# Optimization experiments

Measured on AMD Instinct MI355X. Metric: run time of the kernel, lower is better.

## Reference

```python
import jax, jax.numpy as jnp
import numpy as np

B, Q_LEN, HIST = 1, 2048, 2048
H, KVH, D, HID = 12, 2, 128, 1536
GROUPS = H // KVH  # 6
THETA = 1000000.0


def setup_inputs() -> dict:
    key = jax.random.key(0)
    ks = jax.random.split(key, 8)
    x = jax.random.normal(ks[0], (B, Q_LEN, HID), jnp.float32)
    Wq = jax.random.normal(ks[1], (HID, HID), jnp.float32) * 0.02
    bq = jnp.zeros((HID,), jnp.float32)
    Wk = jax.random.normal(ks[2], (HID, KVH * D), jnp.float32) * 0.02
    bk = jnp.zeros((KVH * D,), jnp.float32)
    Wv = jax.random.normal(ks[3], (HID, KVH * D), jnp.float32) * 0.02
    bv = jnp.zeros((KVH * D,), jnp.float32)
    Wo = jax.random.normal(ks[4], (HID, HID), jnp.float32) * 0.02
    k_hist = jax.random.normal(ks[5], (B, HIST, KVH, D), jnp.float32)
    v_hist = jax.random.normal(ks[6], (B, HIST, KVH, D), jnp.float32)
    # RoPE angles for current-chunk positions [HIST, HIST+Q_LEN)
    inv_freq = 1.0 / (THETA ** (jnp.arange(0, D, 2, dtype=jnp.float32) / D))  # [D/2]
    t = jnp.arange(HIST, HIST + Q_LEN, dtype=jnp.float32)
    ang = t[:, None] * inv_freq[None, :]  # [Q_LEN, D/2]
    return dict(x=x, Wq=Wq, bq=bq, Wk=Wk, bk=bk, Wv=Wv, bv=bv, Wo=Wo,
                k_hist=k_hist, v_hist=v_hist,
                freqs_cos=jnp.cos(ang), freqs_sin=jnp.sin(ang))


def apply_rope(x, cos, sin):
    # x: [B, S, H, D]; cos/sin: [S, D/2]. Split-half rotation (matches torch.polar impl).
    half = D // 2
    x1, x2 = x[..., :half], x[..., half:]
    c = cos[None, :, None, :]
    s = sin[None, :, None, :]
    return jnp.concatenate([x1 * c - x2 * s, x1 * s + x2 * c], axis=-1)


def reference(x, Wq, bq, Wk, bk, Wv, bv, Wo, k_hist, v_hist, freqs_cos, freqs_sin):
    q = (x @ Wq + bq).reshape(B, Q_LEN, H, D)
    k = (x @ Wk + bk).reshape(B, Q_LEN, KVH, D)
    v = (x @ Wv + bv).reshape(B, Q_LEN, KVH, D)
    q = apply_rope(q, freqs_cos, freqs_sin)
    k = apply_rope(k, freqs_cos, freqs_sin)
    # KV-cache concat along sequence dim
    k = jnp.concatenate([k_hist, k], axis=1)  # [B, K_LEN, KVH, D]
    v = jnp.concatenate([v_hist, v], axis=1)
    k_len = HIST + Q_LEN
    # GQA: repeat kv heads (repeat_interleave equivalent along head axis)
    k = jnp.repeat(k, GROUPS, axis=2)  # [B, K_LEN, H, D]
    v = jnp.repeat(v, GROUPS, axis=2)
    scores = jnp.einsum('bqhd,bkhd->bhqk', q, k) / jnp.sqrt(jnp.float32(D))
    # causal mask: triu(-inf, diagonal=k_len - q_len + 1)
    qi = jnp.arange(Q_LEN)[:, None]
    ki = jnp.arange(k_len)[None, :]
    mask = jnp.where(ki > qi + (k_len - Q_LEN), jnp.float32(-jnp.inf), 0.0)
    scores = scores + mask[None, None]
    probs = jax.nn.softmax(scores, axis=-1)
    out = jnp.einsum('bhqk,bkhd->bqhd', probs, v).reshape(B, Q_LEN, HID)
    return out @ Wo
```

## Files before the change

### kernel.cpp

```cpp
#include <hip/hip_runtime.h>
#include <math.h>

#define QL 2048
#define HISTN 2048
#define KLEN 4096
#define NH 12
#define NKVH 2
#define HD 128
#define HID 1536
#define NQKV 2048
#define VTROWS 144
#define QSCALE 0.08838834764831845f

typedef unsigned short u16;
typedef short bf16x8 __attribute__((ext_vector_type(8)));
typedef float f32x4 __attribute__((ext_vector_type(4)));

__device__ __forceinline__ u16 f2bf(float f) {
  union { float f; unsigned u; } v; v.f = f;
  unsigned r = v.u + 0x7FFFu + ((v.u >> 16) & 1u);
  return (u16)(r >> 16);
}
__device__ __forceinline__ float bf2f(u16 h) {
  union { unsigned u; float f; } v; v.u = ((unsigned)h) << 16; return v.f;
}
__device__ __forceinline__ unsigned cvt_pk_bf16(float lo, float hi) {
  unsigned d;
  asm("v_cvt_pk_bf16_f32 %0, %1, %2" : "=v"(d) : "v"(lo), "v"(hi));
  return d;
}

__device__ __forceinline__ void split_T_tile(const float* __restrict__ W,
    u16* __restrict__ BtH, u16* __restrict__ BtL, int K, int N, int k0, int n0,
    int t, float (*T)[65]) {
  const int r = t >> 4, c = (t & 15) * 4;
#pragma unroll
  for (int p = 0; p < 4; ++p) {
    float4 v = *(const float4*)&W[(size_t)(k0 + p * 16 + r) * N + n0 + c];
    T[p * 16 + r][c + 0] = v.x; T[p * 16 + r][c + 1] = v.y;
    T[p * 16 + r][c + 2] = v.z; T[p * 16 + r][c + 3] = v.w;
  }
  __syncthreads();
  const int rr = t >> 2, cc0 = (t & 3) * 16;
#pragma unroll
  for (int i4 = 0; i4 < 4; ++i4) {
    float f0 = T[cc0 + i4 * 4 + 0][rr];
    float f1 = T[cc0 + i4 * 4 + 1][rr];
    float f2 = T[cc0 + i4 * 4 + 2][rr];
    float f3 = T[cc0 + i4 * 4 + 3][rr];
    ushort4 h, l;
    h.x = f2bf(f0); l.x = f2bf(f0 - bf2f(h.x));
    h.y = f2bf(f1); l.y = f2bf(f1 - bf2f(h.y));
    h.z = f2bf(f2); l.z = f2bf(f2 - bf2f(h.z));
    h.w = f2bf(f3); l.w = f2bf(f3 - bf2f(h.w));
    size_t off = (size_t)(n0 + rr) * K + k0 + cc0 + i4 * 4;
    *(ushort4*)&BtH[off] = h;
    *(ushort4*)&BtL[off] = l;
  }
}

__global__ __launch_bounds__(256) void prep(
    const float* __restrict__ x,  const float* __restrict__ Wq,
    const float* __restrict__ Wk, const float* __restrict__ Wv,
    const float* __restrict__ Wo, const float* __restrict__ bq,
    const float* __restrict__ bk, const float* __restrict__ bv,
    u16* __restrict__ xh, u16* __restrict__ xl,
    u16* __restrict__ WqkvH, u16* __restrict__ WqkvL,
    u16* __restrict__ WoH, u16* __restrict__ WoL, float* __restrict__ bcat) {
  __shared__ float T[64][65];
  const int bx = blockIdx.x, t = threadIdx.x;
  if (bx < 3072) {
    int i = bx * 256 + t;
    float4 v = ((const float4*)x)[i];
    ushort4 h, l;
    h.x = f2bf(v.x); l.x = f2bf(v.x - bf2f(h.x));
    h.y = f2bf(v.y); l.y = f2bf(v.y - bf2f(h.y));
    h.z = f2bf(v.z); l.z = f2bf(v.z - bf2f(h.z));
    h.w = f2bf(v.w); l.w = f2bf(v.w - bf2f(h.w));
    ((ushort4*)xh)[i] = h;
    ((ushort4*)xl)[i] = l;
  } else if (bx < 3648) {
    int b = bx - 3072;
    split_T_tile(Wq, WqkvH, WqkvL, HID, HID, (b / 24) * 64, (b % 24) * 64, t, T);
  } else if (bx < 3744) {
    int b = bx - 3648;
    split_T_tile(Wk, WqkvH + (size_t)HID * HID, WqkvL + (size_t)HID * HID,
                 HID, 256, (b / 4) * 64, (b % 4) * 64, t, T);
  } else if (bx < 3840) {
    int b = bx - 3744;
    split_T_tile(Wv, WqkvH + (size_t)(HID + 256) * HID, WqkvL + (size_t)(HID + 256) * HID,
                 HID, 256, (b / 4) * 64, (b % 4) * 64, t, T);
  } else if (bx < 4416) {
    int b = bx - 3840;
    split_T_tile(Wo, WoH, WoL, HID, HID, (b / 24) * 64, (b % 24) * 64, t, T);
  } else {
    int i = (bx - 4416) * 256 + t;
    bcat[i] = (i < HID) ? bq[i] : (i < HID + 256 ? bk[i - HID] : bv[i - HID - 256]);
  }
}

__global__ __launch_bounds__(256, 2) void gemm3(
    const u16* __restrict__ Ah, const u16* __restrict__ Al,
    const u16* __restrict__ Bh, const u16* __restrict__ Bl,
    const float* __restrict__ bias, float* __restrict__ C,
    int K, int ldc) {
  __shared__ __align__(16) u16 sAh[128 * 64];
  __shared__ __align__(16) u16 sAl[128 * 64];
  __shared__ __align__(16) u16 sBh[64 * 64];
  __shared__ __align__(16) u16 sBl[64 * 64];
  const int m0 = blockIdx.y * 128, n0 = blockIdx.x * 64;
  const int t = threadIdx.x, lane = t & 63, w = t >> 6;
  const int quad = lane >> 4, l15 = lane & 15;
  const int wm = w >> 1, wn = w & 1;
  const int l8 = lane >> 3, j8 = lane & 7;

  f32x4 acc[4][2];
#pragma unroll
  for (int mt = 0; mt < 4; ++mt)
#pragma unroll
    for (int nt = 0; nt < 2; ++nt) acc[mt][nt] = (f32x4){0.f, 0.f, 0.f, 0.f};

  for (int k0 = 0; k0 < K; k0 += 64) {
    if (k0) __syncthreads();
#pragma unroll
    for (int i = 0; i < 4; ++i) {
      int r = (i * 4 + w) * 8 + l8;
      size_t goff = (size_t)(m0 + r) * K + k0 + ((j8 ^ (r & 7)) << 3);
      __builtin_amdgcn_global_load_lds(
          (const __attribute__((address_space(1))) void*)(Ah + goff),
          (__attribute__((address_space(3))) void*)&sAh[(i * 4 + w) * 512], 16, 0, 0);
      __builtin_amdgcn_global_load_lds(
          (const __attribute__((address_space(1))) void*)(Al + goff),
          (__attribute__((address_space(3))) void*)&sAl[(i * 4 + w) * 512], 16, 0, 0);
    }
#pragma unroll
    for (int i = 0; i < 2; ++i) {
      int r = (i * 4 + w) * 8 + l8;
      size_t goff = (size_t)(n0 + r) * K + k0 + ((j8 ^ (r & 7)) << 3);
      __builtin_amdgcn_global_load_lds(
          (const __attribute__((address_space(1))) void*)(Bh + goff),
          (__attribute__((address_space(3))) void*)&sBh[(i * 4 + w) * 512], 16, 0, 0);
      __builtin_amdgcn_global_load_lds(
          (const __attribute__((address_space(1))) void*)(Bl + goff),
          (__attribute__((address_space(3))) void*)&sBl[(i * 4 + w) * 512], 16, 0, 0);
    }
    __syncthreads();
#pragma unroll
    for (int kk = 0; kk < 2; ++kk) {
      bf16x8 aH[4], aL[4], bH[2], bL[2];
#pragma unroll
      for (int mt = 0; mt < 4; ++mt) {
        int r = wm * 64 + mt * 16 + l15;
        int addr = r * 64 + ((((kk << 2) + quad) ^ (r & 7)) << 3);
        aH[mt] = *(const bf16x8*)&sAh[addr];
        aL[mt] = *(const bf16x8*)&sAl[addr];
      }
#pragma unroll
      for (int nt = 0; nt < 2; ++nt) {
        int r = wn * 32 + nt * 16 + l15;
        int addr = r * 64 + ((((kk << 2) + quad) ^ (r & 7)) << 3);
        bH[nt] = *(const bf16x8*)&sBh[addr];
        bL[nt] = *(const bf16x8*)&sBl[addr];
      }
#pragma unroll
      for (int mt = 0; mt < 4; ++mt)
#pragma unroll
        for (int nt = 0; nt < 2; ++nt) {
          acc[mt][nt] = __builtin_amdgcn_mfma_f32_16x16x32_bf16(aH[mt], bH[nt], acc[mt][nt], 0, 0, 0);
          acc[mt][nt] = __builtin_amdgcn_mfma_f32_16x16x32_bf16(aH[mt], bL[nt], acc[mt][nt], 0, 0, 0);
          acc[mt][nt] = __builtin_amdgcn_mfma_f32_16x16x32_bf16(aL[mt], bH[nt], acc[mt][nt], 0, 0, 0);
        }
    }
  }
#pragma unroll
  for (int nt = 0; nt < 2; ++nt) {
    int col = n0 + wn * 32 + nt * 16 + l15;
    float bv = bias ? bias[col] : 0.f;
#pragma unroll
    for (int mt = 0; mt < 4; ++mt)
#pragma unroll
      for (int reg = 0; reg < 4; ++reg) {
        int row = m0 + wm * 64 + mt * 16 + quad * 4 + reg;
        C[(size_t)row * ldc + col] = acc[mt][nt][reg] + bv;
      }
  }
}

__global__ __launch_bounds__(256) void post(
    const float* __restrict__ qkv, const float* __restrict__ k_hist,
    const float* __restrict__ v_hist, const float* __restrict__ cs,
    const float* __restrict__ sn, u16* __restrict__ Qb, u16* __restrict__ Kb,
    u16* __restrict__ Vt) {
  __shared__ u16 T[64][68];
  const int bx = blockIdx.x, t = threadIdx.x;
  if (bx < 1536) {
    int idx = bx * 256 + t;
    int dp4 = (idx & 15) * 4;
    int q   = (idx >> 4) & 2047;
    int h   = idx >> 15;
    const float* base = qkv + (size_t)q * NQKV + h * HD;
    float4 x1 = *(const float4*)&base[dp4];
    float4 x2 = *(const float4*)&base[dp4 + 64];
    float4 c = *(const float4*)&cs[q * 64 + dp4];
    float4 s = *(const float4*)&sn[q * 64 + dp4];
    u16* ob = Qb + ((size_t)h * QL + q) * HD;
    ushort4 o1, o2;
    o1.x = f2bf((x1.x * c.x - x2.x * s.x) * QSCALE);
    o1.y = f2bf((x1.y * c.y - x2.y * s.y) * QSCALE);
    o1.z = f2bf((x1.z * c.z - x2.z * s.z) * QSCALE);
    o1.w = f2bf((x1.w * c.w - x2.w * s.w) * QSCALE);
    o2.x = f2bf((x1.x * s.x + x2.x * c.x) * QSCALE);
    o2.y = f2bf((x1.y * s.y + x2.y * c.y) * QSCALE);
    o2.z = f2bf((x1.z * s.z + x2.z * c.z) * QSCALE);
    o2.w = f2bf((x1.w * s.w + x2.w * c.w) * QSCALE);
    *(ushort4*)&ob[dp4]      = o1;
    *(ushort4*)&ob[dp4 + 64] = o2;
  } else if (bx < 2048) {
    int idx = (bx - 1536) * 256 + t;
    int dp4 = (idx & 15) * 4;
    int tt  = (idx >> 4) & 4095;
    int kvh = idx >> 16;
    u16* ob = Kb + ((size_t)kvh * KLEN + tt) * HD;
    if (tt < HISTN) {
      const float* hb = k_hist + ((size_t)tt * NKVH + kvh) * HD;
      float4 a = *(const float4*)&hb[dp4];
      float4 b = *(const float4*)&hb[dp4 + 64];
      ushort4 o1, o2;
      o1.x = f2bf(a.x); o1.y = f2bf(a.y); o1.z = f2bf(a.z); o1.w = f2bf(a.w);
      o2.x = f2bf(b.x); o2.y = f2bf(b.y); o2.z = f2bf(b.z); o2.w = f2bf(b.w);
      *(ushort4*)&ob[dp4]      = o1;
      *(ushort4*)&ob[dp4 + 64] = o2;
    } else {
      int q = tt - HISTN;
      const float* base = qkv + (size_t)q * NQKV + HID + kvh * HD;
      float4 x1 = *(const float4*)&base[dp4];
      float4 x2 = *(const float4*)&base[dp4 + 64];
      float4 c = *(const float4*)&cs[q * 64 + dp4];
      float4 s = *(const float4*)&sn[q * 64 + dp4];
      ushort4 o1, o2;
      o1.x = f2bf(x1.x * c.x - x2.x * s.x);
      o1.y = f2bf(x1.y * c.y - x2.y * s.y);
      o1.z = f2bf(x1.z * c.z - x2.z * s.z);
      o1.w = f2bf(x1.w * c.w - x2.w * s.w);
      o2.x = f2bf(x1.x * s.x + x2.x * c.x);
      o2.y = f2bf(x1.y * s.y + x2.y * c.y);
      o2.z = f2bf(x1.z * s.z + x2.z * c.z);
      o2.w = f2bf(x1.w * s.w + x2.w * c.w);
      *(ushort4*)&ob[dp4]      = o1;
      *(ushort4*)&ob[dp4 + 64] = o2;
    }
  } else {
    int b = bx - 2048;
    int xt = b % 65, rest = b / 65;
    int dh = rest & 1, kvh = rest >> 1;
    if (xt == 64) {
      int r0 = 128 + dh * 8;
      u16* base = Vt + ((size_t)kvh * VTROWS) * KLEN;
      for (int i = t; i < 8192; i += 256) {
        int row = r0 + (i >> 10), c4 = (i & 1023) * 4;
        u16 v = (row == 128) ? (u16)0x3F80 : (u16)0;
        ushort4 o4 = {v, v, v, v};
        *(ushort4*)&base[(size_t)row * KLEN + c4] = o4;
      }
      return;
    }
    const int t0 = xt * 64, d0 = dh * 64;
    const int r = t >> 4, c = (t & 15) * 4;
#pragma unroll
    for (int p = 0; p < 4; ++p) {
      int tt = t0 + p * 16 + r;
      float4 v;
      if (tt < HISTN) v = *(const float4*)&v_hist[((size_t)tt * NKVH + kvh) * HD + d0 + c];
      else            v = *(const float4*)&qkv[(size_t)(tt - HISTN) * NQKV + HID + 256 + kvh * HD + d0 + c];
      T[p * 16 + r][c + 0] = f2bf(v.x); T[p * 16 + r][c + 1] = f2bf(v.y);
      T[p * 16 + r][c + 2] = f2bf(v.z); T[p * 16 + r][c + 3] = f2bf(v.w);
    }
    __syncthreads();
    const int dr = t >> 2, cc0 = (t & 3) * 16;
#pragma unroll
    for (int i4 = 0; i4 < 4; ++i4) {
      ushort4 o4;
      o4.x = T[cc0 + i4 * 4 + 0][dr];
      o4.y = T[cc0 + i4 * 4 + 1][dr];
      o4.z = T[cc0 + i4 * 4 + 2][dr];
      o4.w = T[cc0 + i4 * 4 + 3][dr];
      *(ushort4*)&Vt[((size_t)kvh * VTROWS + d0 + dr) * KLEN + t0 + cc0 + i4 * 4] = o4;
    }
  }
}

__global__ __launch_bounds__(384, 3) void attn6(
    const u16* __restrict__ Q, const u16* __restrict__ K,
    const u16* __restrict__ Vt, float* __restrict__ oacc) {
  __shared__ __align__(16) u16 sK[2][64 * 128];
  __shared__ __align__(16) u16 sV[2][128 * 64];
  const int bid = blockIdx.x;
  const int kvh   = (bid >> 2) & 1;
  const int qs    = (bid & 3) | ((bid >> 3) << 2);
  const int qt    = qs >> 2, slice = qs & 3;
  const int q0 = qt * 32;
  const int t = threadIdx.x, lane = t & 63, w = t / 64;
  const int h = kvh * 6 + w;
  const int quad = lane >> 4, l15 = lane & 15, q8 = quad * 8;

  const u16* Qg = Q + ((size_t)h * QL + q0) * HD;
  bf16x8 Qf[2][4];
#pragma unroll
  for (int mt = 0; mt < 2; ++mt)
#pragma unroll
    for (int dc = 0; dc < 4; ++dc)
      Qf[mt][dc] = *(const bf16x8*)&Qg[(mt * 16 + l15) * HD + dc * 32 + q8];

  const int nsteps = (q0 + 32 + HISTN + 63) >> 6;
  const int bas = nsteps >> 2, rem = nsteps & 3;
  const int cnt = bas + (slice < rem ? 1 : 0);
  const int s0  = slice * bas + (slice < rem ? slice : rem);

  f32x4 o[2][8];
  float lp[2] = {0.f, 0.f};
#pragma unroll
  for (int mt = 0; mt < 2; ++mt)
#pragma unroll
    for (int dt = 0; dt < 8; ++dt) o[mt][dt] = (f32x4){0.f, 0.f, 0.f, 0.f};

  const u16* Kh = K + (size_t)kvh * KLEN * HD;
  const u16* Vh = Vt + (size_t)kvh * VTROWS * KLEN;
  const int x7 = l15 & 7;

  auto STAGE = [&](int b, int k0) {
    for (int i = w; i < 32; i += 6) {
      if (i < 16) {
        int r = 4 * i + (lane >> 4);
        int c = lane & 15;
        const u16* src = Kh + (size_t)(k0 + r) * HD + ((c ^ (r & 7)) << 3);
        __builtin_amdgcn_global_load_lds(
            (const __attribute__((address_space(1))) void*)src,
            (__attribute__((address_space(3))) void*)&sK[b][i * 512], 16, 0, 0);
      } else {
        int j = i - 16;
        int r = 8 * j + (lane >> 3);
        int c = lane & 7;
        const u16* src = Vh + (size_t)r * KLEN + k0 + ((c ^ (r & 7)) << 3);
        __builtin_amdgcn_global_load_lds(
            (const __attribute__((address_space(1))) void*)src,
            (__attribute__((address_space(3))) void*)&sV[b][j * 512], 16, 0, 0);
      }
    }
  };

  int cur = 0;
  STAGE(0, s0 << 6);
  __syncthreads();

  for (int s = s0; s < s0 + cnt; ++s) {
    const int k0 = s << 6;
    if (s + 1 < s0 + cnt) STAGE(cur ^ 1, (s + 1) << 6);
    f32x4 sc[2][4];
#pragma unroll
    for (int mt = 0; mt < 2; ++mt)
#pragma unroll
      for (int kt = 0; kt < 4; ++kt) sc[mt][kt] = (f32x4){0.f, 0.f, 0.f, 0.f};
#pragma unroll
    for (int dc = 0; dc < 4; ++dc) {
      bf16x8 bK[4];
#pragma unroll
      for (int kt = 0; kt < 4; ++kt)
        bK[kt] = *(const bf16x8*)&sK[cur][(kt * 16 + l15) * 128 + (((dc * 4 + quad) ^ x7) << 3)];
#pragma unroll
      for (int mt = 0; mt < 2; ++mt)
#pragma unroll
        for (int kt = 0; kt < 4; ++kt)
          sc[mt][kt] = __builtin_amdgcn_mfma_f32_16x16x32_bf16(bK[kt], Qf[mt][dc], sc[mt][kt], 0, 0, 0);
    }
    if (k0 + 63 - HISTN > q0) {
#pragma unroll
      for (int mt = 0; mt < 2; ++mt)
#pragma unroll
        for (int kt = 0; kt < 4; ++kt) {
#pragma unroll
          for (int reg = 0; reg < 4; ++reg) {
            int kg = k0 + kt * 16 + quad * 4 + reg;
            if (kg > q0 + mt * 16 + l15 + HISTN) sc[mt][kt][reg] = -INFINITY;
          }
        }
    }
#pragma unroll
    for (int mt = 0; mt < 2; ++mt)
#pragma unroll
      for (int kt = 0; kt < 4; ++kt)
#pragma unroll
        for (int reg = 0; reg < 4; ++reg) {
          float p = __expf(sc[mt][kt][reg]);
          sc[mt][kt][reg] = p;
          lp[mt] += p;
        }
#pragma unroll
    for (int kc = 0; kc < 2; ++kc) {
      bf16x8 pP[2];
#pragma unroll
      for (int mt = 0; mt < 2; ++mt) {
        const f32x4 pa = sc[mt][kc * 2];
        const f32x4 pb = sc[mt][kc * 2 + 1];
        unsigned A0 = cvt_pk_bf16(pa[0], pa[1]);
        unsigned A1 = cvt_pk_bf16(pa[2], pa[3]);
        unsigned B0 = cvt_pk_bf16(pb[0], pb[1]);
        unsigned B1 = cvt_pk_bf16(pb[2], pb[3]);
        bool hiQ = quad >= 2;
        unsigned s16a = hiQ ? B0 : A0, s16b = hiQ ? B1 : A1;
        unsigned s3a  = hiQ ? A0 : B0, s3b  = hiQ ? A1 : B1;
        unsigned r16a = __shfl_xor(s16a, 16), r16b = __shfl_xor(s16b, 16);
        unsigned r32a = __shfl_xor(s3a, 32),  r32b = __shfl_xor(s3b, 32);
        unsigned r48a = __shfl_xor(s3a, 48),  r48b = __shfl_xor(s3b, 48);
        union { unsigned u[4]; bf16x8 v; } P;
        P.u[0] = quad == 0 ? A0 : quad == 1 ? r48a : quad == 2 ? r32a : r16a;
        P.u[1] = quad == 0 ? A1 : quad == 1 ? r48b : quad == 2 ? r32b : r16b;
        P.u[2] = quad == 0 ? r16a : quad == 1 ? r32a : quad == 2 ? r48a : B0;
        P.u[3] = quad == 0 ? r16b : quad == 1 ? r32b : quad == 2 ? r48b : B1;
        pP[mt] = P.v;
      }
#pragma unroll
      for (int dt = 0; dt < 8; ++dt) {
        bf16x8 bV = *(const bf16x8*)&sV[cur][(dt * 16 + l15) * 64 + (((kc * 4 + quad) ^ x7) << 3)];
#pragma unroll
        for (int mt = 0; mt < 2; ++mt)
          o[mt][dt] = __builtin_amdgcn_mfma_f32_16x16x32_bf16(bV, pP[mt], o[mt][dt], 0, 0, 0);
      }
    }
    __syncthreads();
    cur ^= 1;
  }

  float* ob = oacc + (size_t)h * 132 * QL + q0;
#pragma unroll
  for (int mt = 0; mt < 2; ++mt) {
    lp[mt] += __shfl_xor(lp[mt], 16);
    lp[mt] += __shfl_xor(lp[mt], 32);
    int qc = mt * 16 + l15;
#pragma unroll
    for (int dt = 0; dt < 8; ++dt)
#pragma unroll
      for (int reg = 0; reg < 4; ++reg)
        atomicAdd(&ob[(size_t)(dt * 16 + quad * 4 + reg) * QL + qc], o[mt][dt][reg]);
    if (quad == 0) atomicAdd(&ob[(size_t)128 * QL + qc], lp[mt]);
  }
}

__global__ __launch_bounds__(256) void attn_norm(const float* __restrict__ oacc,
    u16* __restrict__ OH, u16* __restrict__ OL) {
  __shared__ float T2[128][33];
  __shared__ float linv[32];
  const int h  = blockIdx.x >> 6;
  const int q0 = (blockIdx.x & 63) * 32;
  const int t  = threadIdx.x;
  const float* base = oacc + (size_t)h * 132 * QL + q0;
  const int col = t & 31, r0 = t >> 5;
#pragma unroll
  for (int pass = 0; pass < 16; ++pass) {
    int row = pass * 8 + r0;
    T2[row][col] = base[(size_t)row * QL + col];
  }
  if (t < 32) linv[t] = 1.f / base[(size_t)128 * QL + t];
  __syncthreads();
  const int ql = t >> 3, d0 = (t & 7) * 16;
  float inv = linv[ql];
  size_t ob = (size_t)(q0 + ql) * HID + h * HD + d0;
#pragma unroll
  for (int j = 0; j < 16; ++j) {
    float val = T2[d0 + j][ql] * inv;
    u16 hv = f2bf(val);
    OH[ob + j] = hv;
    OL[ob + j] = f2bf(val - bf2f(hv));
  }
}

extern "C" void kernel_launch(void* const* d_in, const int* in_sizes, int n_in,
                              void* d_out, int out_size, void* d_ws, size_t ws_size,
                              hipStream_t stream) {
  (void)in_sizes; (void)n_in; (void)out_size; (void)ws_size;
  const float* x      = (const float*)d_in[0];
  const float* Wq     = (const float*)d_in[1];
  const float* bq     = (const float*)d_in[2];
  const float* Wk     = (const float*)d_in[3];
  const float* bk     = (const float*)d_in[4];
  const float* Wv     = (const float*)d_in[5];
  const float* bv     = (const float*)d_in[6];
  const float* Wo     = (const float*)d_in[7];
  const float* k_hist = (const float*)d_in[8];
  const float* v_hist = (const float*)d_in[9];
  const float* fcos   = (const float*)d_in[10];
  const float* fsin   = (const float*)d_in[11];
  float* out = (float*)d_out;

  char* p = (char*)d_ws;
  float* qkv   = (float*)p;  p += (size_t)QL * NQKV * 4;
  u16*   Qb    = (u16*)p;    p += (size_t)NH * QL * HD * 2;
  u16*   Kb    = (u16*)p;    p += (size_t)NKVH * KLEN * HD * 2;
  u16*   Vtb   = (u16*)p;    p += (size_t)NKVH * VTROWS * KLEN * 2;
  u16*   xh    = (u16*)p;    p += (size_t)QL * HID * 2;
  u16*   xl    = (u16*)p;    p += (size_t)QL * HID * 2;
  u16*   WqkvH = (u16*)p;    p += (size_t)NQKV * HID * 2;
  u16*   WqkvL = (u16*)p;    p += (size_t)NQKV * HID * 2;
  u16*   WoH   = (u16*)p;    p += (size_t)HID * HID * 2;
  u16*   WoL   = (u16*)p;    p += (size_t)HID * HID * 2;
  float* bcat  = (float*)p;  p += (size_t)NQKV * 4;
  u16* attnH = xh;  u16* attnL = xl;
  float* oacc = qkv;

  prep<<<4424, 256, 0, stream>>>(x, Wq, Wk, Wv, Wo, bq, bk, bv,
                                 xh, xl, WqkvH, WqkvL, WoH, WoL, bcat);
  gemm3<<<dim3(NQKV / 64, QL / 128), 256, 0, stream>>>(xh, xl, WqkvH, WqkvL, bcat, qkv, HID, NQKV);
  post<<<2308, 256, 0, stream>>>(qkv, k_hist, v_hist, fcos, fsin, Qb, Kb, Vtb);
  hipMemsetAsync(oacc, 0, (size_t)NH * 132 * QL * 4, stream);
  attn6<<<512, 384, 0, stream>>>(Qb, Kb, Vtb, oacc);
  attn_norm<<<768, 256, 0, stream>>>(oacc, attnH, attnL);
  gemm3<<<dim3(HID / 64, QL / 128), 256, 0, stream>>>(attnH, attnL, WoH, WoL, nullptr, out, HID, HID);
}
```

Measured before the change: 297.6 us.

## Double-buffer gemm3 LDS tiles with K-step 32 and raise occupancy

Converts the split-bf16 GEMM main loop from a single 64-wide K tile to two 32-wide LDS buffers, so the global-to-LDS load of the next tile is issued while MFMAs run on the current one. The swizzle is rewritten for 32-element rows, and launch bounds are raised to target 3 blocks per CU since LDS use stays the same. The loop takes twice as many iterations, each with a barrier and less work per barrier. Higher occupancy may cause register pressure or spills.

Result: slower. 328.0 us (+10.2%).

```diff
diff --git a/kernel.cpp b/kernel.cpp
--- a/kernel.cpp
+++ b/kernel.cpp
@@ -99,20 +99,21 @@
   }
 }
 
-__global__ __launch_bounds__(256, 2) void gemm3(
+#define SWZ(r) (((r) & 3) ^ (((r) >> 2) & 1))
+__global__ __launch_bounds__(256, 3) void gemm3(
     const u16* __restrict__ Ah, const u16* __restrict__ Al,
     const u16* __restrict__ Bh, const u16* __restrict__ Bl,
     const float* __restrict__ bias, float* __restrict__ C,
     int K, int ldc) {
-  __shared__ __align__(16) u16 sAh[128 * 64];
-  __shared__ __align__(16) u16 sAl[128 * 64];
-  __shared__ __align__(16) u16 sBh[64 * 64];
-  __shared__ __align__(16) u16 sBl[64 * 64];
+  __shared__ __align__(16) u16 sAh[2][128 * 32];
+  __shared__ __align__(16) u16 sAl[2][128 * 32];
+  __shared__ __align__(16) u16 sBh[2][64 * 32];
+  __shared__ __align__(16) u16 sBl[2][64 * 32];
   const int m0 = blockIdx.y * 128, n0 = blockIdx.x * 64;
   const int t = threadIdx.x, lane = t & 63, w = t >> 6;
   const int quad = lane >> 4, l15 = lane & 15;
   const int wm = w >> 1, wn = w & 1;
-  const int l8 = lane >> 3, j8 = lane & 7;
+  const int l4 = lane >> 2, j4 = lane & 3;
 
   f32x4 acc[4][2];
 #pragma unroll
@@ -120,57 +121,61 @@
 #pragma unroll
     for (int nt = 0; nt < 2; ++nt) acc[mt][nt] = (f32x4){0.f, 0.f, 0.f, 0.f};
 
-  for (int k0 = 0; k0 < K; k0 += 64) {
-    if (k0) __syncthreads();
-#pragma unroll
-    for (int i = 0; i < 4; ++i) {
-      int r = (i * 4 + w) * 8 + l8;
-      size_t goff = (size_t)(m0 + r) * K + k0 + ((j8 ^ (r & 7)) << 3);
+  auto STAGE = [&](int b, int k0) {
+#pragma unroll
+    for (int i = 0; i < 2; ++i) {
+      int r = (i * 4 + w) * 16 + l4;
+      size_t goff = (size_t)(m0 + r) * K + k0 + ((j4 ^ SWZ(r)) << 3);
       __builtin_amdgcn_global_load_lds(
           (const __attribute__((address_space(1))) void*)(Ah + goff),
-          (__attribute__((address_space(3))) void*)&sAh[(i * 4 + w) * 512], 16, 0, 0);
+          (__attribute__((address_space(3))) void*)&sAh[b][(i * 4 + w) * 512], 16, 0, 0);
       __builtin_amdgcn_global_load_lds(
           (const __attribute__((address_space(1))) void*)(Al + goff),
-          (__attribute__((address_space(3))) void*)&sAl[(i * 4 + w) * 512], 16, 0, 0);
-    }
-#pragma unroll
-    for (int i = 0; i < 2; ++i) {
-      int r = (i * 4 + w) * 8 + l8;
-      size_t goff = (size_t)(n0 + r) * K + k0 + ((j8 ^ (r & 7)) << 3);
+          (__attribute__((address_space(3))) void*)&sAl[b][(i * 4 + w) * 512], 16, 0, 0);
+    }
+    {
+      int r = w * 16 + l4;
+      size_t goff = (size_t)(n0 + r) * K + k0 + ((j4 ^ SWZ(r)) << 3);
       __builtin_amdgcn_global_load_lds(
           (const __attribute__((address_space(1))) void*)(Bh + goff),
-          (__attribute__((address_space(3))) void*)&sBh[(i * 4 + w) * 512], 16, 0, 0);
+          (__attribute__((address_space(3))) void*)&sBh[b][w * 512], 16, 0, 0);
       __builtin_amdgcn_global_load_lds(
           (const __attribute__((address_space(1))) void*)(Bl + goff),
-          (__attribute__((address_space(3))) void*)&sBl[(i * 4 + w) * 512], 16, 0, 0);
-    }
+          (__attribute__((address_space(3))) void*)&sBl[b][w * 512], 16, 0, 0);
+    }
+  };
+
+  int cur = 0;
+  STAGE(0, 0);
+  __syncthreads();
+
+  for (int k0 = 0; k0 < K; k0 += 32) {
+    if (k0 + 32 < K) STAGE(cur ^ 1, k0 + 32);
+    bf16x8 aH[4], aL[4], bH[2], bL[2];
+#pragma unroll
+    for (int mt = 0; mt < 4; ++mt) {
+      int r = wm * 64 + mt * 16 + l15;
+      int addr = r * 32 + ((quad ^ SWZ(r)) << 3);
+      aH[mt] = *(const bf16x8*)&sAh[cur][addr];
+      aL[mt] = *(const bf16x8*)&sAl[cur][addr];
+    }
+#pragma unroll
+    for (int nt = 0; nt < 2; ++nt) {
+      int r = wn * 32 + nt * 16 + l15;
+      int addr = r * 32 + ((quad ^ SWZ(r)) << 3);
+      bH[nt] = *(const bf16x8*)&sBh[cur][addr];
+      bL[nt] = *(const bf16x8*)&sBl[cur][addr];
+    }
+#pragma unroll
+    for (int mt = 0; mt < 4; ++mt)
+#pragma unroll
+      for (int nt = 0; nt < 2; ++nt) {
+        acc[mt][nt] = __builtin_amdgcn_mfma_f32_16x16x32_bf16(aH[mt], bH[nt], acc[mt][nt], 0, 0, 0);
+        acc[mt][nt] = __builtin_amdgcn_mfma_f32_16x16x32_bf16(aH[mt], bL[nt], acc[mt][nt], 0, 0, 0);
+        acc[mt][nt] = __builtin_amdgcn_mfma_f32_16x16x32_bf16(aL[mt], bH[nt], acc[mt][nt], 0, 0, 0);
+      }
     __syncthreads();
-#pragma unroll
-    for (int kk = 0; kk < 2; ++kk) {
-      bf16x8 aH[4], aL[4], bH[2], bL[2];
-#pragma unroll
-      for (int mt = 0; mt < 4; ++mt) {
-        int r = wm * 64 + mt * 16 + l15;
-        int addr = r * 64 + ((((kk << 2) + quad) ^ (r & 7)) << 3);
-        aH[mt] = *(const bf16x8*)&sAh[addr];
-        aL[mt] = *(const bf16x8*)&sAl[addr];
-      }
-#pragma unroll
-      for (int nt = 0; nt < 2; ++nt) {
-        int r = wn * 32 + nt * 16 + l15;
-        int addr = r * 64 + ((((kk << 2) + quad) ^ (r & 7)) << 3);
-        bH[nt] = *(const bf16x8*)&sBh[addr];
-        bL[nt] = *(const bf16x8*)&sBl[addr];
-      }
-#pragma unroll
-      for (int mt = 0; mt < 4; ++mt)
-#pragma unroll
-        for (int nt = 0; nt < 2; ++nt) {
-          acc[mt][nt] = __builtin_amdgcn_mfma_f32_16x16x32_bf16(aH[mt], bH[nt], acc[mt][nt], 0, 0, 0);
-          acc[mt][nt] = __builtin_amdgcn_mfma_f32_16x16x32_bf16(aH[mt], bL[nt], acc[mt][nt], 0, 0, 0);
-          acc[mt][nt] = __builtin_amdgcn_mfma_f32_16x16x32_bf16(aL[mt], bH[nt], acc[mt][nt], 0, 0, 0);
-        }
-    }
+    cur ^= 1;
   }
 #pragma unroll
   for (int nt = 0; nt < 2; ++nt) {
```
